# Kernel optimization log

Measured on AMD Instinct MI355X. Metric: run time of the kernel, lower is better.

Reference implementation:

```python
import jax, jax.numpy as jnp
import numpy as np

B, T, D = 16, 2048, 256
WINDOW = 128


def setup_inputs() -> dict:
    key = jax.random.key(0)
    ks = jax.random.split(key, 6)
    scale = 1.0 / np.sqrt(D)
    return {
        "x": jax.random.normal(ks[0], (B, T, D), dtype=jnp.float32),
        "Wq": jax.random.normal(ks[1], (D, D), dtype=jnp.float32) * scale,
        "Wk": jax.random.normal(ks[2], (D, D), dtype=jnp.float32) * scale,
        "Wv": jax.random.normal(ks[3], (D, D), dtype=jnp.float32) * scale,
        "Wo": jax.random.normal(ks[4], (D, D), dtype=jnp.float32) * scale,
        "w_bias": jax.random.normal(ks[5], (T, T), dtype=jnp.float32) * 0.1,
        "window": WINDOW,
    }


def reference(x, Wq, Wk, Wv, Wo, w_bias, window):
    # x: [B,T,D]; w_bias: [T,T] learned pairwise position bias.
    T_ = x.shape[1]
    q = jnp.einsum("btd,de->bte", x, Wq)
    k = jnp.einsum("btd,de->bte", x, Wk)
    v = jnp.einsum("btd,de->bte", x, Wv)

    # AFT-Local: bias is zeroed outside the local band |t - t'| < window,
    # but ALL positions still contribute (with bias 0) to the weighted sum.
    idx = jnp.arange(T_)
    band = jnp.abs(idx[:, None] - idx[None, :]) < window  # [T,T] bool
    w_local = jnp.where(band, w_bias, 0.0)

    # Stable exponentials: the num/den ratio is invariant to per-row shifts
    # of w and per-(b,d) shifts of k.
    w_stable = w_local - jnp.max(w_local, axis=1, keepdims=True)
    k_stable = k - jnp.max(k, axis=1, keepdims=True)
    expw = jnp.exp(w_stable)  # [T,T]
    expk = jnp.exp(k_stable)  # [B,T,D]

    num = jnp.einsum("ts,bsd->btd", expw, expk * v)
    den = jnp.einsum("ts,bsd->btd", expw, expk)
    y = jax.nn.sigmoid(q) * (num / den)
    return jnp.einsum("btd,de->bte", y, Wo)
```

## Files before the change

### kernel.cpp

```cpp
#include <hip/hip_runtime.h>
#include <math.h>

#define B_ 16
#define T_ 2048
#define D_ 256
#define W_ 128
#define M_ (B_*T_)

typedef __attribute__((ext_vector_type(8))) short bf16x8;
typedef __attribute__((ext_vector_type(4))) float f32x4;
typedef unsigned short u16;

static __device__ __forceinline__ u16 f32_bf16_rne(float f) {
    unsigned int u = __float_as_uint(f);
    u += 0x7FFF + ((u >> 16) & 1);
    return (u16)(u >> 16);
}
static __device__ __forceinline__ float bf16_f32(u16 h) {
    return __uint_as_float(((unsigned int)h) << 16);
}
static __device__ __forceinline__ void gload_lds16(const u16* g, u16* l) {
    __builtin_amdgcn_global_load_lds(
        (const __attribute__((address_space(1))) void*)g,
        (__attribute__((address_space(3))) void*)l, 16, 0, 0);
}

__global__ __launch_bounds__(256) void aft_split_wT(
    const float* __restrict__ Wq, const float* __restrict__ Wk,
    const float* __restrict__ Wv, const float* __restrict__ Wo,
    u16* __restrict__ Wth, u16* __restrict__ Wkl)
{
    __shared__ alignas(16) u16 Th[64][72];
    __shared__ alignas(16) u16 Tl[64][72];
    const float* Ws[4] = {Wq, Wk, Wv, Wo};
    const int mat = blockIdx.x;
    const float* W = Ws[mat];
    const int k0 = (blockIdx.y & 3) * 64;
    const int n0 = (blockIdx.y >> 2) * 64;
    const int tid = threadIdx.x;

    #pragma unroll
    for (int p = 0; p < 4; ++p) {
        const int k = p * 16 + (tid >> 4);
        const int n = (tid & 15) * 4;
        float4 v = *(const float4*)&W[(size_t)(k0 + k) * 256 + n0 + n];
        float vv[4] = {v.x, v.y, v.z, v.w};
        #pragma unroll
        for (int e = 0; e < 4; ++e) {
            u16 h = f32_bf16_rne(vv[e]);
            Th[n + e][k] = h;
            Tl[n + e][k] = f32_bf16_rne(vv[e] - bf16_f32(h));
        }
    }
    __syncthreads();

    const int n  = tid >> 2;
    const int kc = (tid & 3) * 16;
    size_t ob = ((size_t)mat * 256 + n0 + n) * 256 + k0 + kc;
    *(uint4*)&Wth[ob]     = *(const uint4*)&Th[n][kc];
    *(uint4*)&Wth[ob + 8] = *(const uint4*)&Th[n][kc + 8];
    if (mat == 1) {
        size_t ol = ((size_t)(n0 + n)) * 256 + k0 + kc;
        *(uint4*)&Wkl[ol]     = *(const uint4*)&Tl[n][kc];
        *(uint4*)&Wkl[ol + 8] = *(const uint4*)&Tl[n][kc + 8];
    }
}

__global__ void aft_ewb(const float* __restrict__ wb, u16* __restrict__ EWb)
{
    const int t = blockIdx.x;
    const int j = threadIdx.x;
    const int s = (t & ~63) - 128 + j;
    const int dlt = s - t;
    float v = 0.f;
    if (s >= 0 && s < T_ && dlt > -W_ && dlt < W_)
        v = expf(wb[(size_t)t * T_ + s]) - 1.0f;
    EWb[(size_t)t * 320 + j] = f32_bf16_rne(v);
}

__global__ __launch_bounds__(256, 3) void aft_qkv_mfma(
    const float* __restrict__ x,
    const u16* __restrict__ Wth, const u16* __restrict__ Wkl,
    u16* __restrict__ ekT, u16* __restrict__ sigqT)
{
    __shared__ alignas(16) u16 sm[12288];
    u16* Ah = sm;
    u16* Al = sm + 2048;
    u16* Bs = sm + 4096;
    u16* Tr = sm;

    const int tid  = threadIdx.x;
    const int row0 = blockIdx.x * 64;
    const int col0 = blockIdx.y * 64;
    const int b    = row0 >> 11;
    const int t0g  = row0 & (T_ - 1);
    const int lane = tid & 63;
    const int wid  = tid >> 6;
    const int wm   = (wid >> 1) * 32;
    const int wn   = (wid & 1) * 32;
    const int qd   = lane >> 4;
    const int r    = lane & 15;

    f32x4 accq[2][2], acck[2][2], accv[2][2];
    #pragma unroll
    for (int i = 0; i < 2; ++i)
        #pragma unroll
        for (int j = 0; j < 2; ++j) {
            accq[i][j] = (f32x4){0.f, 0.f, 0.f, 0.f};
            acck[i][j] = accq[i][j];
            accv[i][j] = accq[i][j];
        }

    const int crow  = tid >> 2;
    const int gchk  = tid & 3;
    const int cswz  = (crow >> 1) & 3;
    const int ccols = (gchk ^ cswz) * 8;
    const int aslot = crow * 32 + (gchk ^ cswz) * 8;
    const int wbase = wid * 512;
    const int sq8   = (qd ^ ((r >> 1) & 3)) * 8;

    for (int k0 = 0; k0 < D_; k0 += 32) {
        if (k0) __syncthreads();
        {
            size_t gb = (size_t)(col0 + crow) * 256 + k0 + ccols;
            gload_lds16(&Wth[gb],          &Bs[0 * 2048 + wbase]);
            gload_lds16(&Wth[65536 + gb],  &Bs[1 * 2048 + wbase]);
            gload_lds16(&Wkl[gb],          &Bs[2 * 2048 + wbase]);
            gload_lds16(&Wth[131072 + gb], &Bs[3 * 2048 + wbase]);
        }
        {
            size_t ga = (size_t)(row0 + crow) * 256 + k0 + gchk * 8;
            float4 v0 = *(const float4*)&x[ga];
            float4 v1 = *(const float4*)&x[ga + 4];
            float vv[8] = {v0.x, v0.y, v0.z, v0.w, v1.x, v1.y, v1.z, v1.w};
            union { uint4 q; u16 h[8]; } H, L;
            #pragma unroll
            for (int e = 0; e < 8; ++e) {
                u16 h = f32_bf16_rne(vv[e]);
                H.h[e] = h;
                L.h[e] = f32_bf16_rne(vv[e] - bf16_f32(h));
            }
            *(uint4*)&Ah[aslot] = H.q;
            *(uint4*)&Al[aslot] = L.q;
        }
        __syncthreads();

        bf16x8 ah[2], al[2];
        #pragma unroll
        for (int mf = 0; mf < 2; ++mf) {
            int ar = (wm + mf * 16 + r) * 32 + sq8;
            ah[mf] = *(const bf16x8*)&Ah[ar];
            al[mf] = *(const bf16x8*)&Al[ar];
        }
        #pragma unroll
        for (int nf = 0; nf < 2; ++nf) {
            int br = (wn + nf * 16 + r) * 32 + sq8;
            bf16x8 bq  = *(const bf16x8*)&Bs[br];
            bf16x8 bkh = *(const bf16x8*)&Bs[2048 + br];
            bf16x8 bkl = *(const bf16x8*)&Bs[4096 + br];
            bf16x8 bv  = *(const bf16x8*)&Bs[6144 + br];
            #pragma unroll
            for (int mf = 0; mf < 2; ++mf) {
                accq[mf][nf] = __builtin_amdgcn_mfma_f32_16x16x32_bf16(ah[mf], bq,  accq[mf][nf], 0, 0, 0);
                acck[mf][nf] = __builtin_amdgcn_mfma_f32_16x16x32_bf16(ah[mf], bkh, acck[mf][nf], 0, 0, 0);
                acck[mf][nf] = __builtin_amdgcn_mfma_f32_16x16x32_bf16(ah[mf], bkl, acck[mf][nf], 0, 0, 0);
                acck[mf][nf] = __builtin_amdgcn_mfma_f32_16x16x32_bf16(al[mf], bkh, acck[mf][nf], 0, 0, 0);
                accv[mf][nf] = __builtin_amdgcn_mfma_f32_16x16x32_bf16(ah[mf], bv,  accv[mf][nf], 0, 0, 0);
            }
        }
    }

    const int dl_r = tid >> 2;
    const int tseg = (tid & 3) * 16;
    #pragma unroll
    for (int round = 0; round < 3; ++round) {
        __syncthreads();
        #pragma unroll
        for (int mf = 0; mf < 2; ++mf) {
            #pragma unroll
            for (int nf = 0; nf < 2; ++nf) {
                ushort4 o;
                float vals[4];
                #pragma unroll
                for (int reg = 0; reg < 4; ++reg) {
                    if (round == 0)      vals[reg] = expf(acck[mf][nf][reg]);
                    else if (round == 1) vals[reg] = expf(acck[mf][nf][reg]) * accv[mf][nf][reg];
                    else                 vals[reg] = 1.f / (1.f + expf(-accq[mf][nf][reg]));
                }
                o.x = f32_bf16_rne(vals[0]); o.y = f32_bf16_rne(vals[1]);
                o.z = f32_bf16_rne(vals[2]); o.w = f32_bf16_rne(vals[3]);
                int dl = wn + nf * 16 + r;
                int tt = wm + mf * 16 + qd * 4;
                *(ushort4*)&Tr[dl * 72 + tt] = o;
            }
        }
        __syncthreads();
        u16* dst;
        if (round == 0)      dst = ekT   + ((size_t)(b * 512 + col0 + dl_r)) * 2048;
        else if (round == 1) dst = ekT   + ((size_t)(b * 512 + 256 + col0 + dl_r)) * 2048;
        else                 dst = sigqT + ((size_t)(b * 256 + col0 + dl_r)) * 2048;
        dst += t0g + tseg;
        const u16* srcp = &Tr[dl_r * 72 + tseg];
        *(uint4*)&dst[0] = *(const uint4*)&srcp[0];
        *(uint4*)&dst[8] = *(const uint4*)&srcp[8];
    }
}

__global__ __launch_bounds__(256) void aft_sums(
    const u16* __restrict__ ekT, float* __restrict__ Sk, float* __restrict__ Sv)
{
    const int wid  = threadIdx.x >> 6;
    const int lane = threadIdx.x & 63;
    const int row  = blockIdx.x * 4 + wid;
    const int b = row >> 9, n = row & 511;
    const u16* p = ekT + (size_t)row * 2048 + lane * 32;
    float s = 0.f;
    #pragma unroll
    for (int c = 0; c < 4; ++c) {
        union { uint4 v; u16 h[8]; } u;
        u.v = *(const uint4*)&p[c * 8];
        #pragma unroll
        for (int i = 0; i < 8; ++i) s += bf16_f32(u.h[i]);
    }
    #pragma unroll
    for (int off = 32; off >= 1; off >>= 1) s += __shfl_down(s, off, 64);
    if (lane == 0) {
        if (n < 256) Sk[b * 256 + n] = s;
        else         Sv[b * 256 + n - 256] = s;
    }
}

__global__ __launch_bounds__(256) void aft_band_mfma(
    const u16* __restrict__ EWb, const u16* __restrict__ ekT,
    const u16* __restrict__ sigqT,
    const float* __restrict__ Sk, const float* __restrict__ Sv,
    u16* __restrict__ yTD)
{
    __shared__ alignas(16) u16 sm[12800];
    u16* Aw  = sm;
    u16* Bkv = sm + 2560;

    const int tid  = threadIdx.x;
    const int t0   = blockIdx.x * 64;
    const int b    = blockIdx.y >> 1;
    const int dh   = (blockIdx.y & 1) * 128;
    const int lane = tid & 63;
    const int wid  = tid >> 6;
    const int wn   = wid * 32;
    const int qd   = lane >> 4;
    const int r    = lane & 15;

    f32x4 accn[4][2], accd[4][2];
    #pragma unroll
    for (int i = 0; i < 4; ++i)
        #pragma unroll
        for (int j = 0; j < 2; ++j) {
            accn[i][j] = (f32x4){0.f, 0.f, 0.f, 0.f};
            accd[i][j] = (f32x4){0.f, 0.f, 0.f, 0.f};
        }

    const int atl = tid >> 2;
    const int ak8 = (tid & 3) * 8;

    for (int c = 0; c < 10; ++c) {
        const int sc = t0 - 128 + c * 32;
        if (sc < 0 || sc >= T_) continue;
        __syncthreads();
        *(uint4*)&Aw[atl * 40 + ak8] =
            *(const uint4*)&EWb[(size_t)(t0 + atl) * 320 + c * 32 + ak8];
        #pragma unroll
        for (int rr = 0; rr < 4; ++rr) {
            int nl = rr * 64 + atl;
            int n  = (nl < 128) ? (dh + nl) : (256 + dh + nl - 128);
            *(uint4*)&Bkv[nl * 40 + ak8] =
                *(const uint4*)&ekT[((size_t)(b * 512) + n) * 2048 + sc + ak8];
        }
        __syncthreads();

        bf16x8 af[4];
        #pragma unroll
        for (int mf = 0; mf < 4; ++mf)
            af[mf] = *(const bf16x8*)&Aw[(mf * 16 + r) * 40 + qd * 8];
        #pragma unroll
        for (int nf = 0; nf < 2; ++nf) {
            bf16x8 be = *(const bf16x8*)&Bkv[(wn + nf * 16 + r) * 40 + qd * 8];
            bf16x8 bv = *(const bf16x8*)&Bkv[(128 + wn + nf * 16 + r) * 40 + qd * 8];
            #pragma unroll
            for (int mf = 0; mf < 4; ++mf) {
                accd[mf][nf] = __builtin_amdgcn_mfma_f32_16x16x32_bf16(af[mf], be, accd[mf][nf], 0, 0, 0);
                accn[mf][nf] = __builtin_amdgcn_mfma_f32_16x16x32_bf16(af[mf], bv, accn[mf][nf], 0, 0, 0);
            }
        }
    }

    __syncthreads();
    u16* Ly = sm;
    #pragma unroll
    for (int nf = 0; nf < 2; ++nf) {
        const int dl = wn + nf * 16 + r;
        const int d  = dh + dl;
        const float skq = Sk[(b << 8) + d];
        const float svq = Sv[(b << 8) + d];
        #pragma unroll
        for (int mf = 0; mf < 4; ++mf) {
            const int tt = t0 + mf * 16 + qd * 4;
            size_t off = ((size_t)(b << 8) + d) * 2048 + tt;
            ushort4 sg = *(const ushort4*)&sigqT[off];
            float s4[4] = {bf16_f32(sg.x), bf16_f32(sg.y), bf16_f32(sg.z), bf16_f32(sg.w)};
            #pragma unroll
            for (int reg = 0; reg < 4; ++reg) {
                float y = s4[reg] * (svq + accn[mf][nf][reg]) / (skq + accd[mf][nf][reg]);
                Ly[(mf * 16 + qd * 4 + reg) * 136 + dl] = f32_bf16_rne(y);
            }
        }
    }
    __syncthreads();
    {
        const int tl  = tid >> 2;
        const int ds4 = (tid & 3) * 32;
        u16* dst = yTD + ((size_t)b * 2048 + t0 + tl) * 256 + dh + ds4;
        #pragma unroll
        for (int i = 0; i < 4; ++i)
            *(uint4*)&dst[i * 8] = *(const uint4*)&Ly[tl * 136 + ds4 + i * 8];
    }
}

__global__ __launch_bounds__(256) void aft_out_mfma(
    const u16* __restrict__ yTD, const u16* __restrict__ Woth,
    float* __restrict__ out)
{
    __shared__ alignas(16) u16 sm[7680];
    u16* As = sm;
    u16* Bh = sm + 2560;

    const int tid  = threadIdx.x;
    const int row0 = blockIdx.x * 64;
    const int col0 = blockIdx.y * 128;
    const int lane = tid & 63;
    const int wid  = tid >> 6;
    const int wn   = wid * 32;
    const int qd   = lane >> 4;
    const int r    = lane & 15;

    f32x4 acc[4][2];
    #pragma unroll
    for (int i = 0; i < 4; ++i)
        #pragma unroll
        for (int j = 0; j < 2; ++j)
            acc[i][j] = (f32x4){0.f, 0.f, 0.f, 0.f};

    const int arow = tid >> 2;
    const int aseg = (tid & 3) * 8;
    const int brw  = tid >> 1;
    const int bsg  = (tid & 1) * 16;

    for (int k0 = 0; k0 < D_; k0 += 32) {
        {
            uint4 v = *(const uint4*)&yTD[(size_t)(row0 + arow) * 256 + k0 + aseg];
            *(uint4*)&As[arow * 40 + aseg] = v;
        }
        {
            size_t g = (size_t)(col0 + brw) * 256 + k0 + bsg;
            uint4 v0 = *(const uint4*)&Woth[g];
            uint4 v1 = *(const uint4*)&Woth[g + 8];
            *(uint4*)&Bh[brw * 40 + bsg]     = v0;
            *(uint4*)&Bh[brw * 40 + bsg + 8] = v1;
        }
        __syncthreads();

        bf16x8 af[4];
        #pragma unroll
        for (int mf = 0; mf < 4; ++mf)
            af[mf] = *(const bf16x8*)&As[(mf * 16 + r) * 40 + qd * 8];
        #pragma unroll
        for (int nf = 0; nf < 2; ++nf) {
            bf16x8 bh = *(const bf16x8*)&Bh[(wn + nf * 16 + r) * 40 + qd * 8];
            #pragma unroll
            for (int mf = 0; mf < 4; ++mf)
                acc[mf][nf] = __builtin_amdgcn_mfma_f32_16x16x32_bf16(af[mf], bh, acc[mf][nf], 0, 0, 0);
        }
        __syncthreads();
    }

    #pragma unroll
    for (int mf = 0; mf < 4; ++mf)
        #pragma unroll
        for (int nf = 0; nf < 2; ++nf)
            #pragma unroll
            for (int reg = 0; reg < 4; ++reg) {
                int mrow = row0 + mf * 16 + qd * 4 + reg;
                int ncol = col0 + wn + nf * 16 + r;
                out[(size_t)mrow * D_ + ncol] = acc[mf][nf][reg];
            }
}

extern "C" void kernel_launch(void* const* d_in, const int* in_sizes, int n_in,
                              void* d_out, int out_size, void* d_ws, size_t ws_size,
                              hipStream_t stream)
{
    const float* x  = (const float*)d_in[0];
    const float* Wq = (const float*)d_in[1];
    const float* Wk = (const float*)d_in[2];
    const float* Wv = (const float*)d_in[3];
    const float* Wo = (const float*)d_in[4];
    const float* wb = (const float*)d_in[5];

    u16* Wth   = (u16*)d_ws;
    u16* Wkl   = Wth + 262144;
    u16* EWb   = Wkl + 65536;
    u16* ekT   = EWb + 655360;
    u16* sigqT = ekT + 16777216;
    u16* yTD   = sigqT + 8388608;
    float* Sk  = (float*)(yTD + 8388608);
    float* Sv  = Sk + 4096;

    aft_split_wT<<<dim3(4, 16), 256, 0, stream>>>(Wq, Wk, Wv, Wo, Wth, Wkl);
    aft_ewb<<<dim3(T_), 320, 0, stream>>>(wb, EWb);
    aft_qkv_mfma<<<dim3(M_ / 64, 4), 256, 0, stream>>>(x, Wth, Wkl, ekT, sigqT);
    aft_sums<<<dim3(8192 / 4), 256, 0, stream>>>(ekT, Sk, Sv);
    aft_band_mfma<<<dim3(T_ / 64, B_ * 2), 256, 0, stream>>>(EWb, ekT, sigqT, Sk, Sv, yTD);
    aft_out_mfma<<<dim3(M_ / 64, 2), 256, 0, stream>>>(yTD, Wth + 3 * 65536, (float*)d_out);
}
```

Before: 194.3 us.

## Double-buffer LDS in QKV projection kernel to overlap loads with MFMA

Doubles the shared-memory buffer of the QKV projection GEMM and software-pipelines the K loop. The next chunk's x tile is loaded into registers and the next weight tile is staged into the alternate LDS buffer while MFMAs run on the current one, with manual waitcnt and a single barrier per iteration. This aims to hide global-load latency behind compute. LDS use doubles to 48KB per block, which may lower occupancy below the launch-bounds target of 3 blocks per CU.

```diff
diff --git a/kernel.cpp b/kernel.cpp
--- a/kernel.cpp
+++ b/kernel.cpp
@@ -83,10 +83,7 @@
     const u16* __restrict__ Wth, const u16* __restrict__ Wkl,
     u16* __restrict__ ekT, u16* __restrict__ sigqT)
 {
-    __shared__ alignas(16) u16 sm[12288];
-    u16* Ah = sm;
-    u16* Al = sm + 2048;
-    u16* Bs = sm + 4096;
+    __shared__ alignas(16) u16 sm[24576];
     u16* Tr = sm;
 
     const int tid  = threadIdx.x;
@@ -119,56 +116,86 @@
     const int wbase = wid * 512;
     const int sq8   = (qd ^ ((r >> 1) & 3)) * 8;
 
-    for (int k0 = 0; k0 < D_; k0 += 32) {
-        if (k0) __syncthreads();
-        {
-            size_t gb = (size_t)(col0 + crow) * 256 + k0 + ccols;
-            gload_lds16(&Wth[gb],          &Bs[0 * 2048 + wbase]);
-            gload_lds16(&Wth[65536 + gb],  &Bs[1 * 2048 + wbase]);
-            gload_lds16(&Wkl[gb],          &Bs[2 * 2048 + wbase]);
-            gload_lds16(&Wth[131072 + gb], &Bs[3 * 2048 + wbase]);
-        }
-        {
-            size_t ga = (size_t)(row0 + crow) * 256 + k0 + gchk * 8;
-            float4 v0 = *(const float4*)&x[ga];
-            float4 v1 = *(const float4*)&x[ga + 4];
-            float vv[8] = {v0.x, v0.y, v0.z, v0.w, v1.x, v1.y, v1.z, v1.w};
-            union { uint4 q; u16 h[8]; } H, L;
-            #pragma unroll
-            for (int e = 0; e < 8; ++e) {
-                u16 h = f32_bf16_rne(vv[e]);
-                H.h[e] = h;
-                L.h[e] = f32_bf16_rne(vv[e] - bf16_f32(h));
-            }
-            *(uint4*)&Ah[aslot] = H.q;
-            *(uint4*)&Al[aslot] = L.q;
-        }
-        __syncthreads();
-
-        bf16x8 ah[2], al[2];
-        #pragma unroll
-        for (int mf = 0; mf < 2; ++mf) {
-            int ar = (wm + mf * 16 + r) * 32 + sq8;
-            ah[mf] = *(const bf16x8*)&Ah[ar];
-            al[mf] = *(const bf16x8*)&Al[ar];
-        }
-        #pragma unroll
-        for (int nf = 0; nf < 2; ++nf) {
-            int br = (wn + nf * 16 + r) * 32 + sq8;
-            bf16x8 bq  = *(const bf16x8*)&Bs[br];
-            bf16x8 bkh = *(const bf16x8*)&Bs[2048 + br];
-            bf16x8 bkl = *(const bf16x8*)&Bs[4096 + br];
-            bf16x8 bv  = *(const bf16x8*)&Bs[6144 + br];
-            #pragma unroll
-            for (int mf = 0; mf < 2; ++mf) {
-                accq[mf][nf] = __builtin_amdgcn_mfma_f32_16x16x32_bf16(ah[mf], bq,  accq[mf][nf], 0, 0, 0);
-                acck[mf][nf] = __builtin_amdgcn_mfma_f32_16x16x32_bf16(ah[mf], bkh, acck[mf][nf], 0, 0, 0);
-                acck[mf][nf] = __builtin_amdgcn_mfma_f32_16x16x32_bf16(ah[mf], bkl, acck[mf][nf], 0, 0, 0);
-                acck[mf][nf] = __builtin_amdgcn_mfma_f32_16x16x32_bf16(al[mf], bkh, acck[mf][nf], 0, 0, 0);
-                accv[mf][nf] = __builtin_amdgcn_mfma_f32_16x16x32_bf16(ah[mf], bv,  accv[mf][nf], 0, 0, 0);
-            }
-        }
-    }
+    const size_t xbase = (size_t)(row0 + crow) * 256 + gchk * 8;
+    const size_t wbrow = (size_t)(col0 + crow) * 256 + ccols;
+
+    float4 xa, xb;
+
+#define XLOAD(KK) do {                                                       \
+    xa = *(const float4*)&x[xbase + (KK)];                                   \
+    xb = *(const float4*)&x[xbase + (KK) + 4];                               \
+} while (0)
+
+#define BSTAGE(KK, BOFF) do {                                                \
+    size_t gb_ = wbrow + (KK);                                               \
+    gload_lds16(&Wth[gb_],          &sm[(BOFF) + 4096  + wbase]);            \
+    gload_lds16(&Wth[65536 + gb_],  &sm[(BOFF) + 6144  + wbase]);            \
+    gload_lds16(&Wkl[gb_],          &sm[(BOFF) + 8192  + wbase]);            \
+    gload_lds16(&Wth[131072 + gb_], &sm[(BOFF) + 10240 + wbase]);            \
+} while (0)
+
+#define AWRITE(BOFF) do {                                                    \
+    float vv_[8] = {xa.x, xa.y, xa.z, xa.w, xb.x, xb.y, xb.z, xb.w};         \
+    union { uint4 q; u16 h[8]; } H_, L_;                                     \
+    _Pragma("unroll")                                                        \
+    for (int e_ = 0; e_ < 8; ++e_) {                                         \
+        u16 h_ = f32_bf16_rne(vv_[e_]);                                      \
+        H_.h[e_] = h_;                                                       \
+        L_.h[e_] = f32_bf16_rne(vv_[e_] - bf16_f32(h_));                     \
+    }                                                                        \
+    *(uint4*)&sm[(BOFF) + aslot]        = H_.q;                              \
+    *(uint4*)&sm[(BOFF) + 2048 + aslot] = L_.q;                              \
+} while (0)
+
+#define COMPUTE(BOFF) do {                                                   \
+    bf16x8 ah_[2], al_[2];                                                   \
+    _Pragma("unroll")                                                        \
+    for (int mf = 0; mf < 2; ++mf) {                                         \
+        int ar_ = (wm + mf * 16 + r) * 32 + sq8;                             \
+        ah_[mf] = *(const bf16x8*)&sm[(BOFF) + ar_];                         \
+        al_[mf] = *(const bf16x8*)&sm[(BOFF) + 2048 + ar_];                  \
+    }                                                                        \
+    _Pragma("unroll")                                                        \
+    for (int nf = 0; nf < 2; ++nf) {                                         \
+        int br_ = (wn + nf * 16 + r) * 32 + sq8;                             \
+        bf16x8 bq_  = *(const bf16x8*)&sm[(BOFF) + 4096  + br_];             \
+        bf16x8 bkh_ = *(const bf16x8*)&sm[(BOFF) + 6144  + br_];             \
+        bf16x8 bkl_ = *(const bf16x8*)&sm[(BOFF) + 8192  + br_];             \
+        bf16x8 bv_  = *(const bf16x8*)&sm[(BOFF) + 10240 + br_];             \
+        _Pragma("unroll")                                                    \
+        for (int mf = 0; mf < 2; ++mf) {                                     \
+            accq[mf][nf] = __builtin_amdgcn_mfma_f32_16x16x32_bf16(ah_[mf], bq_,  accq[mf][nf], 0, 0, 0); \
+            acck[mf][nf] = __builtin_amdgcn_mfma_f32_16x16x32_bf16(ah_[mf], bkh_, acck[mf][nf], 0, 0, 0); \
+            acck[mf][nf] = __builtin_amdgcn_mfma_f32_16x16x32_bf16(ah_[mf], bkl_, acck[mf][nf], 0, 0, 0); \
+            acck[mf][nf] = __builtin_amdgcn_mfma_f32_16x16x32_bf16(al_[mf], bkh_, acck[mf][nf], 0, 0, 0); \
+            accv[mf][nf] = __builtin_amdgcn_mfma_f32_16x16x32_bf16(ah_[mf], bv_,  accv[mf][nf], 0, 0, 0); \
+        }                                                                    \
+    }                                                                        \
+} while (0)
+
+    XLOAD(0);
+    BSTAGE(0, 0);
+
+    #pragma unroll
+    for (int ks = 0; ks < 8; ++ks) {
+        const int cur = (ks & 1) * 12288;
+        const int nxt = 12288 - cur;
+        AWRITE(cur);
+        if (ks < 7) {
+            XLOAD((ks + 1) * 32);
+            asm volatile("s_waitcnt vmcnt(2) lgkmcnt(0)" ::: "memory");
+        } else {
+            asm volatile("s_waitcnt vmcnt(0) lgkmcnt(0)" ::: "memory");
+        }
+        __builtin_amdgcn_s_barrier();
+        __builtin_amdgcn_sched_barrier(0);
+        if (ks < 7) BSTAGE((ks + 1) * 32, nxt);
+        COMPUTE(cur);
+    }
+#undef XLOAD
+#undef BSTAGE
+#undef AWRITE
+#undef COMPUTE
 
     const int dl_r = tid >> 2;
     const int tseg = (tid & 3) * 16;
```

Result: no change. 198.1 us (+2.0%).
